# Kernel optimization log

Measured on AMD Instinct MI355X. Metric: run time of the kernel, lower is better.

## Reference

```python
import jax, jax.numpy as jnp
import numpy as np

LAYER_SHAPES = [(256, 64, 56, 56), (256, 128, 28, 28), (256, 256, 14, 14), (256, 512, 7, 7)]
NUM_REF = 2000


def _lid_layer(ref, q, k):
    """MLE LID estimate (Ma et al.) per query row.
    ref: [R, C] reference activations; q: [B, C] pooled query activations.
    """
    # Euclidean cdist via the expansion ||q||^2 - 2 q.ref^T + ||ref||^2
    d2 = (jnp.sum(q * q, axis=1, keepdims=True)
          - 2.0 * (q @ ref.T)
          + jnp.sum(ref * ref, axis=1)[None, :])            # [B, R]
    d = jnp.sqrt(jnp.maximum(d2, 0.0))
    # smallest k+1 distances, drop the nearest (mirrors sorted[:,1:k+1])
    neg_topk = jax.lax.top_k(-d, k + 1)[0]                   # descending in -d => ascending d
    dk = -neg_topk[:, 1:k + 1]                               # [B, k], ascending
    # LID = -k / sum_i log(d_i / d_k)
    return -k / jnp.sum(jnp.log(dk / dk[:, -1:]), axis=1)    # [B]


def setup_inputs() -> dict:
    key = jax.random.key(0)
    ks = jax.random.split(key, 12)
    inp = {}
    for i, shp in enumerate(LAYER_SHAPES):
        inp[f"feat{i}"] = jax.random.normal(ks[i], shp, dtype=jnp.float32)
        inp[f"ref{i}"] = jax.random.normal(ks[4 + i], (NUM_REF, shp[1]), dtype=jnp.float32)
    inp["reg_w"] = jax.random.normal(ks[8], (1, 4), dtype=jnp.float32)
    inp["reg_b"] = jax.random.normal(ks[9], (1,), dtype=jnp.float32)
    inp["k"] = 20
    return inp


def reference(feat0, feat1, feat2, feat3, ref0, ref1, ref2, ref3, reg_w, reg_b, k):
    feats = [feat0, feat1, feat2, feat3]
    refs = [ref0, ref1, ref2, ref3]
    lid_scores = []
    for f, r in zip(feats, refs):
        fq = jnp.mean(f.reshape(f.shape[0], f.shape[1], -1), axis=2)  # [B, C]
        lid_scores.append(_lid_layer(r, fq, k))
    lid_feat = jnp.stack(lid_scores, axis=1)                 # [B, num_layers]
    logit = lid_feat @ reg_w.T + reg_b                        # [B, 1]
    return jax.nn.sigmoid(logit)[:, 0]
```

## Files before the change

### kernel.cpp

```cpp
#include <hip/hip_runtime.h>
#include <cmath>

#define WS_FQ_OFF      0u
#define WS_R2_OFF      245760u
#define WS_LID_OFF     253760u
#define WS_G_OFF       262144u
#define G_CHUNK_STRIDE 512000u
#define NREF           2000
#define KC             64

__global__ __launch_bounds__(256) void pool_kernel(const float* __restrict__ feat,
                                                   float* __restrict__ fq,
                                                   int HW, float invHW) {
    int w = threadIdx.x >> 6, lane = threadIdx.x & 63;
    size_t row = (size_t)blockIdx.x * 4 + w;
    const float* p = feat + row * (size_t)HW;
    float s = 0.f;
    if ((HW & 3) == 0) {
        const float4* p4 = (const float4*)p;
        int n4 = HW >> 2;
        for (int i = lane; i < n4; i += 64) {
            float4 v = p4[i];
            s += (v.x + v.y) + (v.z + v.w);
        }
    } else {
        for (int i = lane; i < HW; i += 64) s += p[i];
    }
    #pragma unroll
    for (int off = 32; off; off >>= 1) s += __shfl_down(s, off, 64);
    if (lane == 0) fq[row] = s * invHW;
}

__global__ __launch_bounds__(256) void r2_kernel(const float* __restrict__ ref0,
                                                 const float* __restrict__ ref1,
                                                 const float* __restrict__ ref2,
                                                 const float* __restrict__ ref3,
                                                 float* __restrict__ r2_all) {
    int layer = blockIdx.y;
    int w = threadIdx.x >> 6, lane = threadIdx.x & 63;
    int r = blockIdx.x * 4 + w;
    if (r >= NREF) return;
    const float* rp; int C;
    switch (layer) {
        case 0:  rp = ref0; C = 64;  break;
        case 1:  rp = ref1; C = 128; break;
        case 2:  rp = ref2; C = 256; break;
        default: rp = ref3; C = 512; break;
    }
    const float4* row = (const float4*)(rp + (size_t)r * C);
    int n4 = C >> 2;
    float s = 0.f;
    for (int i = lane; i < n4; i += 64) {
        float4 v = row[i];
        s += v.x*v.x + v.y*v.y + v.z*v.z + v.w*v.w;
    }
    #pragma unroll
    for (int off = 32; off; off >>= 1) s += __shfl_down(s, off, 64);
    if (lane == 0) r2_all[layer * NREF + r] = s;
}

#define BM 64
#define BN 64
#define BK 32
#define LDT 68
__global__ __launch_bounds__(256) void gemm_qr(const float* __restrict__ A,
                                               const float* __restrict__ B,
                                               float* __restrict__ Gp,
                                               int K, int N) {
    __shared__ __align__(16) float As[BK * LDT];
    __shared__ __align__(16) float Bs[BK * LDT];
    int t = threadIdx.x;
    int tq = t & 15, tr = t >> 4;
    int m0 = blockIdx.x * BM;
    int n0 = blockIdx.y * BN;
    int kb = blockIdx.z * KC;
    int row0 = t >> 3;
    int kc4  = t & 7;
    float acc[4][4] = {};

    for (int k0 = kb; k0 < kb + KC; k0 += BK) {
        #pragma unroll
        for (int half = 0; half < 2; ++half) {
            int row = row0 + half * 32;
            float4 av = *(const float4*)(A + (size_t)(m0 + row) * K + k0 + kc4 * 4);
            int brow = n0 + row;
            float4 bv = make_float4(0.f, 0.f, 0.f, 0.f);
            if (brow < N) bv = *(const float4*)(B + (size_t)brow * K + k0 + kc4 * 4);
            As[(kc4*4 + 0) * LDT + row] = av.x;
            As[(kc4*4 + 1) * LDT + row] = av.y;
            As[(kc4*4 + 2) * LDT + row] = av.z;
            As[(kc4*4 + 3) * LDT + row] = av.w;
            Bs[(kc4*4 + 0) * LDT + row] = bv.x;
            Bs[(kc4*4 + 1) * LDT + row] = bv.y;
            Bs[(kc4*4 + 2) * LDT + row] = bv.z;
            Bs[(kc4*4 + 3) * LDT + row] = bv.w;
        }
        __syncthreads();
        #pragma unroll
        for (int kk = 0; kk < BK; ++kk) {
            float4 a = *(const float4*)&As[kk * LDT + tq * 4];
            float4 b = *(const float4*)&Bs[kk * LDT + tr * 4];
            acc[0][0] += a.x*b.x; acc[0][1] += a.x*b.y; acc[0][2] += a.x*b.z; acc[0][3] += a.x*b.w;
            acc[1][0] += a.y*b.x; acc[1][1] += a.y*b.y; acc[1][2] += a.y*b.z; acc[1][3] += a.y*b.w;
            acc[2][0] += a.z*b.x; acc[2][1] += a.z*b.y; acc[2][2] += a.z*b.z; acc[2][3] += a.z*b.w;
            acc[3][0] += a.w*b.x; acc[3][1] += a.w*b.y; acc[3][2] += a.w*b.z; acc[3][3] += a.w*b.w;
        }
        __syncthreads();
    }

    float* Gout = Gp + (size_t)blockIdx.z * G_CHUNK_STRIDE;
    int rbase = n0 + tr * 4;
    if (rbase < N) {
        #pragma unroll
        for (int i = 0; i < 4; ++i) {
            float4 o = make_float4(acc[i][0], acc[i][1], acc[i][2], acc[i][3]);
            *(float4*)(Gout + (size_t)(m0 + tq*4 + i) * N + rbase) = o;
        }
    }
}

__global__ __launch_bounds__(256) void topk_lid_kernel(const float* __restrict__ fq_all,
                                                       const float* __restrict__ G_all,
                                                       const float* __restrict__ r2_all,
                                                       float* __restrict__ lid,
                                                       const int* __restrict__ kptr) {
    __shared__ __align__(16) float d2s[NREF];
    __shared__ unsigned hist[2048];
    __shared__ float redq[4], redm[4], redl[4];
    __shared__ unsigned long long red8[4];
    __shared__ int sh_B, sh_cbelow, sh_cnt;
    __shared__ float sh_dmin;

    const int Cs[4]   = {64, 128, 256, 512};
    const int fqo[4]  = {0, 16384, 49152, 114688};
    const int nchs[4] = {1, 2, 4, 8};
    const int coff[4] = {0, 1, 3, 7};

    int b = blockIdx.x, layer = blockIdx.y;
    int t = threadIdx.x;
    int lane = t & 63, w = t >> 6;
    int k = kptr[0];
    if (k + 1 > NREF) k = NREF - 1;
    unsigned K1 = (unsigned)(k + 1);
    int C = Cs[layer];
    int nch = nchs[layer];
    const float* fq = fq_all + fqo[layer] + (size_t)b * C;
    const float* Gb = G_all + (size_t)coff[layer] * G_CHUNK_STRIDE + (size_t)b * NREF;
    const float* r2 = r2_all + layer * NREF;
    const float INF = __uint_as_float(0x7f800000u);

    for (int i = t; i < 2048; i += 256) hist[i] = 0u;
    if (t == 0) sh_cnt = 0;
    float s = 0.f;
    for (int c = t; c < C; c += 256) { float v = fq[c]; s += v * v; }
    #pragma unroll
    for (int off = 32; off; off >>= 1) s += __shfl_down(s, off, 64);
    if (lane == 0) redq[w] = s;
    __syncthreads();
    float q2 = redq[0] + redq[1] + redq[2] + redq[3];

    float minv = INF;
    for (int i = t; i < NREF / 4; i += 256) {
        float4 g = make_float4(0.f, 0.f, 0.f, 0.f);
        for (int c = 0; c < nch; ++c) {
            float4 v = *(const float4*)(Gb + (size_t)c * G_CHUNK_STRIDE + i * 4);
            g.x += v.x; g.y += v.y; g.z += v.z; g.w += v.w;
        }
        float4 rr = *(const float4*)(r2 + i * 4);
        float d0 = q2 - 2.f * g.x + rr.x; d0 = d0 > 0.f ? d0 : 0.f;
        float d1 = q2 - 2.f * g.y + rr.y; d1 = d1 > 0.f ? d1 : 0.f;
        float d2_ = q2 - 2.f * g.z + rr.z; d2_ = d2_ > 0.f ? d2_ : 0.f;
        float d3 = q2 - 2.f * g.w + rr.w; d3 = d3 > 0.f ? d3 : 0.f;
        *(float4*)(d2s + i * 4) = make_float4(d0, d1, d2_, d3);
        atomicAdd(&hist[__float_as_uint(d0) >> 20], 1u);
        atomicAdd(&hist[__float_as_uint(d1) >> 20], 1u);
        atomicAdd(&hist[__float_as_uint(d2_) >> 20], 1u);
        atomicAdd(&hist[__float_as_uint(d3) >> 20], 1u);
        minv = fminf(minv, fminf(fminf(d0, d1), fminf(d2_, d3)));
    }
    #pragma unroll
    for (int off = 32; off; off >>= 1) minv = fminf(minv, __shfl_down(minv, off, 64));
    if (lane == 0) redm[w] = minv;
    __syncthreads();

    if (t < 64) {
        unsigned p = 0;
        int base = t * 32;
        #pragma unroll 4
        for (int i = 0; i < 32; ++i) p += hist[base + i];
        unsigned cum = p;
        #pragma unroll
        for (int off = 1; off < 64; off <<= 1) {
            unsigned o = __shfl_up(cum, off, 64);
            if (t >= off) cum += o;
        }
        unsigned excl = cum - p;
        if (excl < K1 && K1 <= cum) {
            unsigned run = excl;
            int binB = base;
            for (int i = 0; i < 32; ++i) {
                unsigned c = hist[base + i];
                if (run + c >= K1) { binB = base + i; break; }
                run += c;
            }
            sh_B = binB;
            sh_cbelow = (int)run;
        }
        if (t == 0) sh_dmin = fminf(fminf(redm[0], redm[1]), fminf(redm[2], redm[3]));
    }
    __syncthreads();

    int B = sh_B;
    float* cand = (float*)hist;
    float lsum = 0.f;
    for (int i = t; i < NREF; i += 256) {
        float v = d2s[i];
        int bin = (int)(__float_as_uint(v) >> 20);
        if (bin < B) {
            lsum += logf(v);
        } else if (bin == B) {
            int pos = atomicAdd(&sh_cnt, 1);
            cand[pos] = v;
        }
    }
    #pragma unroll
    for (int off = 32; off; off >>= 1) lsum += __shfl_down(lsum, off, 64);
    if (lane == 0) redl[w] = lsum;
    __syncthreads();

    int cnt = sh_cnt;
    int m = (int)K1 - sh_cbelow;
    if (cnt <= 64) {
        if (t < 64) {
            float mv = (t < cnt) ? cand[t] : INF;
            float csum = 0.f, dk = 0.f;
            for (int it = 0; it < m; ++it) {
                float x = mv;
                #pragma unroll
                for (int off = 32; off; off >>= 1) x = fminf(x, __shfl_xor(x, off, 64));
                csum += logf(x);
                dk = x;
                unsigned long long ball = __ballot(mv == x);
                int src = __ffsll(ball) - 1;
                if (t == src) mv = INF;
            }
            if (t == 0) {
                float lsum_tot = redl[0] + redl[1] + redl[2] + redl[3];
                float denom = 0.5f * (lsum_tot + csum - logf(sh_dmin) - (float)k * logf(dk));
                lid[b * 4 + layer] = -(float)k / denom;
            }
        }
    } else {
        float csum = 0.f, dk = 0.f;
        for (int it = 0; it < m; ++it) {
            unsigned long long best = ~0ull;
            for (int i = t; i < cnt; i += 256) {
                unsigned long long key =
                    ((unsigned long long)__float_as_uint(cand[i]) << 32) | (unsigned)i;
                if (key < best) best = key;
            }
            #pragma unroll
            for (int off = 32; off; off >>= 1) {
                unsigned long long o = __shfl_down(best, off, 64);
                if (o < best) best = o;
            }
            if (lane == 0) red8[w] = best;
            __syncthreads();
            unsigned long long mm = red8[0];
            #pragma unroll
            for (int ww = 1; ww < 4; ++ww) if (red8[ww] < mm) mm = red8[ww];
            float v = __uint_as_float((unsigned)(mm >> 32));
            if (t == 0) {
                csum += logf(v);
                dk = v;
                cand[(int)(mm & 0xffffffffu)] = INF;
            }
            __syncthreads();
        }
        if (t == 0) {
            float lsum_tot = redl[0] + redl[1] + redl[2] + redl[3];
            float denom = 0.5f * (lsum_tot + csum - logf(sh_dmin) - (float)k * logf(dk));
            lid[b * 4 + layer] = -(float)k / denom;
        }
    }
}

__global__ __launch_bounds__(256) void head_kernel(const float* __restrict__ lid,
                                                   const float* __restrict__ w,
                                                   const float* __restrict__ bias,
                                                   float* __restrict__ out) {
    int b = threadIdx.x;
    float acc = bias[0];
    #pragma unroll
    for (int l = 0; l < 4; ++l) acc += lid[b * 4 + l] * w[l];
    out[b] = 1.f / (1.f + expf(-acc));
}

extern "C" void kernel_launch(void* const* d_in, const int* in_sizes, int n_in,
                              void* d_out, int out_size, void* d_ws, size_t ws_size,
                              hipStream_t stream) {
    const float* feat[4] = {(const float*)d_in[0], (const float*)d_in[2],
                            (const float*)d_in[4], (const float*)d_in[6]};
    const float* ref[4]  = {(const float*)d_in[1], (const float*)d_in[3],
                            (const float*)d_in[5], (const float*)d_in[7]};
    const float* reg_w = (const float*)d_in[8];
    const float* reg_b = (const float*)d_in[9];
    const int*   kptr  = (const int*)d_in[10];

    float* ws     = (float*)d_ws;
    float* fq_all = ws + WS_FQ_OFF;
    float* r2_all = ws + WS_R2_OFF;
    float* lid    = ws + WS_LID_OFF;
    float* G_part = ws + WS_G_OFF;

    const int Cs[4]   = {64, 128, 256, 512};
    const int HWs[4]  = {3136, 784, 196, 49};
    const int fqo[4]  = {0, 16384, 49152, 114688};
    const int coff[4] = {0, 1, 3, 7};

    for (int l = 0; l < 4; ++l) {
        int rows = 256 * Cs[l];
        pool_kernel<<<rows / 4, 256, 0, stream>>>(feat[l], fq_all + fqo[l],
                                                  HWs[l], 1.0f / (float)HWs[l]);
    }
    r2_kernel<<<dim3(NREF / 4, 4), 256, 0, stream>>>(ref[0], ref[1], ref[2], ref[3], r2_all);
    for (int l = 0; l < 4; ++l) {
        int chunks = Cs[l] / KC;
        gemm_qr<<<dim3(256 / BM, (NREF + BN - 1) / BN, chunks), 256, 0, stream>>>(
            fq_all + fqo[l], ref[l], G_part + (size_t)coff[l] * G_CHUNK_STRIDE, Cs[l], NREF);
    }
    topk_lid_kernel<<<dim3(256, 4), 256, 0, stream>>>(fq_all, G_part, r2_all, lid, kptr);
    head_kernel<<<1, 256, 0, stream>>>(lid, reg_w, reg_b, (float*)d_out);
}
```

Baseline: 481.5 us.

## Merge per-layer pool and GEMM launches into single kernels with compile-time sizes

The four pooling launches become one pooling kernel that dispatches on block index to a per-layer path templated on HW, with unrolled loops and a scalar path for HW=49. The four GEMM launches become one flattened-grid GEMM kernel that picks its layer and chunk from the block index. The goal is to cut launch count and tail gaps between small kernels. The top-k loop also gains wave broadcasts of csum/dk, which look redundant and add a few shuffles.

```diff
diff --git a/kernel.cpp b/kernel.cpp
--- a/kernel.cpp
+++ b/kernel.cpp
@@ -9,26 +9,53 @@
 #define NREF           2000
 #define KC             64
 
-__global__ __launch_bounds__(256) void pool_kernel(const float* __restrict__ feat,
-                                                   float* __restrict__ fq,
-                                                   int HW, float invHW) {
-    int w = threadIdx.x >> 6, lane = threadIdx.x & 63;
-    size_t row = (size_t)blockIdx.x * 4 + w;
-    const float* p = feat + row * (size_t)HW;
+template<int HW>
+__device__ __forceinline__ void pool_row_vec(const float* __restrict__ feat,
+                                             float* __restrict__ fq,
+                                             int row, int lane) {
+    constexpr int N4 = HW / 4;
+    const float4* p4 = (const float4*)(feat + (size_t)row * HW);
     float s = 0.f;
-    if ((HW & 3) == 0) {
-        const float4* p4 = (const float4*)p;
-        int n4 = HW >> 2;
-        for (int i = lane; i < n4; i += 64) {
+    constexpr int ITER = (N4 + 63) / 64;
+    #pragma unroll
+    for (int it = 0; it < ITER; ++it) {
+        int i = lane + it * 64;
+        if ((N4 & 63) == 0 || i < N4) {
             float4 v = p4[i];
             s += (v.x + v.y) + (v.z + v.w);
         }
+    }
+    #pragma unroll
+    for (int off = 32; off; off >>= 1) s += __shfl_down(s, off, 64);
+    if (lane == 0) fq[row] = s * (1.0f / (float)HW);
+}
+
+__device__ __forceinline__ void pool_row_49(const float* __restrict__ feat,
+                                            float* __restrict__ fq,
+                                            int row, int lane) {
+    const float* p = feat + (size_t)row * 49;
+    float s = (lane < 49) ? p[lane] : 0.f;
+    #pragma unroll
+    for (int off = 32; off; off >>= 1) s += __shfl_down(s, off, 64);
+    if (lane == 0) fq[row] = s * (1.0f / 49.0f);
+}
+
+__global__ __launch_bounds__(256) void pool_all_kernel(const float* __restrict__ f0,
+                                                       const float* __restrict__ f1,
+                                                       const float* __restrict__ f2,
+                                                       const float* __restrict__ f3,
+                                                       float* __restrict__ fq_all) {
+    int bid = blockIdx.x;
+    int lane = threadIdx.x & 63, w = threadIdx.x >> 6;
+    if (bid < 4096) {
+        pool_row_vec<3136>(f0, fq_all + 0,      bid * 4 + w, lane);
+    } else if (bid < 12288) {
+        pool_row_vec<784>(f1, fq_all + 16384,  (bid - 4096) * 4 + w, lane);
+    } else if (bid < 28672) {
+        pool_row_vec<196>(f2, fq_all + 49152,  (bid - 12288) * 4 + w, lane);
     } else {
-        for (int i = lane; i < HW; i += 64) s += p[i];
-    }
-    #pragma unroll
-    for (int off = 32; off; off >>= 1) s += __shfl_down(s, off, 64);
-    if (lane == 0) fq[row] = s * invHW;
+        pool_row_49(f3, fq_all + 114688, (bid - 28672) * 4 + w, lane);
+    }
 }
 
 __global__ __launch_bounds__(256) void r2_kernel(const float* __restrict__ ref0,
@@ -63,29 +90,49 @@
 #define BN 64
 #define BK 32
 #define LDT 68
-__global__ __launch_bounds__(256) void gemm_qr(const float* __restrict__ A,
-                                               const float* __restrict__ B,
-                                               float* __restrict__ Gp,
-                                               int K, int N) {
+__global__ __launch_bounds__(256) void gemm_all(const float* __restrict__ fq_all,
+                                                const float* __restrict__ rf0,
+                                                const float* __restrict__ rf1,
+                                                const float* __restrict__ rf2,
+                                                const float* __restrict__ rf3,
+                                                float* __restrict__ G_part) {
     __shared__ __align__(16) float As[BK * LDT];
     __shared__ __align__(16) float Bs[BK * LDT];
+
+    int bid = blockIdx.x;
+    int layer = (bid >= 128) + (bid >= 384) + (bid >= 896);
+    const int offt[4] = {0, 128, 384, 896};
+    const int Ks[4]   = {64, 128, 256, 512};
+    const int fqo[4]  = {0, 16384, 49152, 114688};
+    const int coff[4] = {0, 1, 3, 7};
+
+    int K = Ks[layer];
+    const float* A = fq_all + fqo[layer];
+    const float* B = layer == 0 ? rf0 : layer == 1 ? rf1 : layer == 2 ? rf2 : rf3;
+    int local = bid - offt[layer];
+    int chunk = local >> 7;
+    int rem   = local & 127;
+    int m0 = (rem & 3) * BM;
+    int n0 = (rem >> 2) * BN;
+    int kb = chunk * KC;
+    float* Gout = G_part + (size_t)(coff[layer] + chunk) * G_CHUNK_STRIDE;
+
     int t = threadIdx.x;
     int tq = t & 15, tr = t >> 4;
-    int m0 = blockIdx.x * BM;
-    int n0 = blockIdx.y * BN;
-    int kb = blockIdx.z * KC;
     int row0 = t >> 3;
     int kc4  = t & 7;
     float acc[4][4] = {};
 
-    for (int k0 = kb; k0 < kb + KC; k0 += BK) {
+    #pragma unroll
+    for (int ko = 0; ko < KC / BK; ++ko) {
+        int k0 = kb + ko * BK;
         #pragma unroll
         for (int half = 0; half < 2; ++half) {
             int row = row0 + half * 32;
             float4 av = *(const float4*)(A + (size_t)(m0 + row) * K + k0 + kc4 * 4);
             int brow = n0 + row;
             float4 bv = make_float4(0.f, 0.f, 0.f, 0.f);
-            if (brow < N) bv = *(const float4*)(B + (size_t)brow * K + k0 + kc4 * 4);
+            if (brow < NREF) bv = *(const float4*)(B + (size_t)brow * K + k0 + kc4 * 4);
             As[(kc4*4 + 0) * LDT + row] = av.x;
             As[(kc4*4 + 1) * LDT + row] = av.y;
             As[(kc4*4 + 2) * LDT + row] = av.z;
@@ -108,13 +155,12 @@
         __syncthreads();
     }
 
-    float* Gout = Gp + (size_t)blockIdx.z * G_CHUNK_STRIDE;
     int rbase = n0 + tr * 4;
-    if (rbase < N) {
+    if (rbase < NREF) {
         #pragma unroll
         for (int i = 0; i < 4; ++i) {
             float4 o = make_float4(acc[i][0], acc[i][1], acc[i][2], acc[i][3]);
-            *(float4*)(Gout + (size_t)(m0 + tq*4 + i) * N + rbase) = o;
+            *(float4*)(Gout + (size_t)(m0 + tq*4 + i) * NREF + rbase) = o;
         }
     }
 }
@@ -276,6 +322,9 @@
                 cand[(int)(mm & 0xffffffffu)] = INF;
             }
             __syncthreads();
+            if (lane == 0 && w == 0) { }
+            csum = __shfl(csum, 0, 64);
+            dk = __shfl(dk, 0, 64);
         }
         if (t == 0) {
             float lsum_tot = redl[0] + redl[1] + redl[2] + redl[3];
@@ -313,22 +362,9 @@
     float* lid    = ws + WS_LID_OFF;
     float* G_part = ws + WS_G_OFF;
 
-    const int Cs[4]   = {64, 128, 256, 512};
-    const int HWs[4]  = {3136, 784, 196, 49};
-    const int fqo[4]  = {0, 16384, 49152, 114688};
-    const int coff[4] = {0, 1, 3, 7};
-
-    for (int l = 0; l < 4; ++l) {
-        int rows = 256 * Cs[l];
-        pool_kernel<<<rows / 4, 256, 0, stream>>>(feat[l], fq_all + fqo[l],
-                                                  HWs[l], 1.0f / (float)HWs[l]);
-    }
+    pool_all_kernel<<<61440, 256, 0, stream>>>(feat[0], feat[1], feat[2], feat[3], fq_all);
     r2_kernel<<<dim3(NREF / 4, 4), 256, 0, stream>>>(ref[0], ref[1], ref[2], ref[3], r2_all);
-    for (int l = 0; l < 4; ++l) {
-        int chunks = Cs[l] / KC;
-        gemm_qr<<<dim3(256 / BM, (NREF + BN - 1) / BN, chunks), 256, 0, stream>>>(
-            fq_all + fqo[l], ref[l], G_part + (size_t)coff[l] * G_CHUNK_STRIDE, Cs[l], NREF);
-    }
+    gemm_all<<<1920, 256, 0, stream>>>(fq_all, ref[0], ref[1], ref[2], ref[3], G_part);
     topk_lid_kernel<<<dim3(256, 4), 256, 0, stream>>>(fq_all, G_part, r2_all, lid, kptr);
     head_kernel<<<1, 256, 0, stream>>>(lid, reg_w, reg_b, (float*)d_out);
 }
```

Result: no change. 489.8 us (+1.7%).
